# Kernel optimization log

Measured on AMD Instinct MI355X. Metric: run time of the kernel, lower is better.

Reference implementation:

```python
import jax, jax.numpy as jnp
import numpy as np

B, T, D = 32, 512, 768
K, H = 256, 512


def setup_inputs() -> dict:
    key = jax.random.key(0)
    ks = jax.random.split(key, 5)
    s = 0.02  # keep pre-activations in a sane range
    return {
        "inputs": jax.random.normal(ks[0], (B, T, D), jnp.float32),
        "W_x": jax.random.normal(ks[1], (K + 1, 4 * H), jnp.float32) * s,
        "W_h": jax.random.normal(ks[2], (H, 4 * H), jnp.float32) * s,
        "b_lstm": jnp.zeros((4 * H,), jnp.float32),
        "W_key": jax.random.normal(ks[3], (H, K), jnp.float32) * s,
        "b_key": jnp.zeros((K,), jnp.float32),
        "W_g": jax.random.normal(ks[4], (H, 1), jnp.float32) * s,
        "b_g": jnp.zeros((1,), jnp.float32),
        "conf_gain": jnp.ones((), jnp.float32),
        "conf_bias": jnp.zeros((), jnp.float32),
    }


def reference(inputs, W_x, W_h, b_lstm, W_key, b_key, W_g, b_g, conf_gain, conf_bias):
    Bq, Tq, Dq = inputs.shape
    Kq = W_key.shape[1]
    Hq = W_h.shape[0]
    t_idx = jnp.arange(Tq)
    xs = jnp.transpose(inputs, (1, 0, 2))  # [T, B, D]

    def step(carry, xt):
        t, x = xt  # t: scalar step index, x: [B, D]
        key_r, h, c, M_k, M_v = carry
        # Keras LSTMCell (gate order i, f, c, o); input is previous key_r [B, K+1]
        z = key_r @ W_x + h @ W_h + b_lstm
        i, f, g_c, o = jnp.split(z, 4, axis=-1)
        i = jax.nn.sigmoid(i)
        f = jax.nn.sigmoid(f)
        g_c = jnp.tanh(g_c)
        o = jax.nn.sigmoid(o)
        c = f * c + i * g_c
        h = o * jnp.tanh(c)  # lstm_out == hidden in Keras LSTMCell
        key_w = h @ W_key + b_key            # [B, K]
        g = jax.nn.sigmoid(h @ W_g + b_g)    # [B, 1]
        # similarity attention over all previously written memory slots
        sim = jnp.einsum('bd,tbd->bt', x, M_v)          # [B, T]
        mask = (t_idx < t)[None, :]                     # valid slots only
        w_k = jax.nn.softmax(jnp.where(mask, sim, -1e30), axis=1)
        c_k = jax.nn.sigmoid(sim * conf_gain + conf_bias)
        aug = jnp.concatenate([jnp.transpose(M_k, (1, 0, 2)), c_k[:, :, None]], axis=2)  # [B, T, K+1]
        key_r_new = jnp.where(t > 0, g * jnp.einsum('bt,btk->bk', w_k, aug), 0.0)
        M_k = M_k.at[t].set(key_w)
        M_v = M_v.at[t].set(x)
        return (key_r_new, h, c, M_k, M_v), None

    init = (
        jnp.zeros((Bq, Kq + 1), inputs.dtype),
        jnp.zeros((Bq, Hq), inputs.dtype),
        jnp.zeros((Bq, Hq), inputs.dtype),
        jnp.zeros((Tq, Bq, Kq), inputs.dtype),
        jnp.zeros((Tq, Bq, Dq), inputs.dtype),
    )
    (key_r, h, c, M_k, M_v), _ = jax.lax.scan(step, init, (t_idx, xs))
    return h  # final lstm_out
```

## Files before the change

kernel.cpp:

```cpp
#include <hip/hip_runtime.h>
#include <math.h>

#define BQ 32
#define TQ 512
#define DQ 768
#define KQ 256
#define HQ 512
#define G4 2048
#define BROW 768
#define STP 772
#define NWG 512
#define NTHR 256
#define NBG 4

typedef float f32x4 __attribute__((ext_vector_type(4)));

__device__ __forceinline__ void waitcnt0() {
  asm volatile("s_waitcnt vmcnt(0) lgkmcnt(0)" ::: "memory");
}
__device__ __forceinline__ void st_dev(float* p, float v) {
  asm volatile("global_store_dword %0, %1, off sc1" :: "v"(p), "v"(v) : "memory");
}
__device__ __forceinline__ int ld_dev(const int* p) {
  int v;
  asm volatile("global_load_dword %0, %1, off sc1\ns_waitcnt vmcnt(0)"
               : "=v"(v) : "v"(p) : "memory");
  return v;
}
__device__ __forceinline__ void wg_wait_ctr(const int* ctr, int target) {
  if (threadIdx.x < 64) {
    while (ld_dev(ctr) < target) __builtin_amdgcn_s_sleep(1);
  }
  __syncthreads();
}
__device__ __forceinline__ void wg_signal_ctr(int* ctr) {
  waitcnt0();
  __syncthreads();
  if (threadIdx.x == 0) atomicAdd(ctr, 1);
}
__device__ __forceinline__ float sigm(float x) { return 1.f / (1.f + __expf(-x)); }

__global__ void __launch_bounds__(256) gram_k(const float* __restrict__ X,
                                              float* __restrict__ Gm) {
  __shared__ __align__(16) float As[64 * 33];
  __shared__ __align__(16) float Bs[64 * 33];
  const int bid = blockIdx.x;
  const int b = blockIdx.y;
  int I = 0, base = 0;
  while (base + I + 1 <= bid) { base += I + 1; ++I; }
  const int J = bid - base;
  const int t0 = I * 64, u0 = J * 64;
  const float* Xb = X + (size_t)b * TQ * DQ;
  const int ty = threadIdx.x >> 4, tx = threadIdx.x & 15;
  const int sc = threadIdx.x & 31, sr = threadIdx.x >> 5;
  float acc[4][4];
#pragma unroll
  for (int i = 0; i < 4; ++i)
#pragma unroll
    for (int j = 0; j < 4; ++j) acc[i][j] = 0.f;
  for (int k0 = 0; k0 < DQ; k0 += 32) {
#pragma unroll
    for (int rr = 0; rr < 8; ++rr) {
      const int r = rr * 8 + sr;
      As[r * 33 + sc] = Xb[(size_t)(t0 + r) * DQ + k0 + sc];
      Bs[r * 33 + sc] = Xb[(size_t)(u0 + r) * DQ + k0 + sc];
    }
    __syncthreads();
#pragma unroll
    for (int k = 0; k < 32; ++k) {
      float av[4], bv[4];
#pragma unroll
      for (int i = 0; i < 4; ++i) av[i] = As[(ty * 4 + i) * 33 + k];
#pragma unroll
      for (int j = 0; j < 4; ++j) bv[j] = Bs[(tx * 4 + j) * 33 + k];
#pragma unroll
      for (int i = 0; i < 4; ++i)
#pragma unroll
        for (int j = 0; j < 4; ++j) acc[i][j] += av[i] * bv[j];
    }
    __syncthreads();
  }
  float* gb = Gm + (size_t)b * TQ * TQ;
#pragma unroll
  for (int i = 0; i < 4; ++i) {
    f32x4 o;
    o.x = acc[i][0]; o.y = acc[i][1]; o.z = acc[i][2]; o.w = acc[i][3];
    *(f32x4*)&gb[(size_t)(t0 + ty * 4 + i) * TQ + u0 + tx * 4] = o;
  }
}

__global__ void __launch_bounds__(256) smax_k(float* __restrict__ Gm,
                                              float* __restrict__ Sv,
                                              const float* __restrict__ cgp,
                                              const float* __restrict__ cbp) {
  const int t = blockIdx.x + 1;
  const int b = blockIdx.y;
  const int tid = threadIdx.x;
  const int lane = tid & 63;
  const int wv = tid >> 6;
  __shared__ float row[TQ];
  __shared__ float r1[4], r2[4], r3[4];
  float* R = Gm + ((size_t)b * TQ + t) * TQ;
  const float cg = cgp[0], cb = cbp[0];
  for (int i = tid; i < t; i += 256) row[i] = R[i];
  __syncthreads();
  float m = -3e38f;
  for (int i = tid; i < t; i += 256) m = fmaxf(m, row[i]);
#pragma unroll
  for (int k = 1; k < 64; k <<= 1) m = fmaxf(m, __shfl_xor(m, k));
  if (lane == 0) r1[wv] = m;
  __syncthreads();
  m = fmaxf(fmaxf(r1[0], r1[1]), fmaxf(r1[2], r1[3]));
  float s = 0.f, sck = 0.f;
  for (int i = tid; i < t; i += 256) {
    const float r = row[i];
    const float e = __expf(r - m);
    const float ck = 1.f / (1.f + __expf(-(r * cg + cb)));
    row[i] = e; s += e; sck += e * ck;
  }
#pragma unroll
  for (int k = 1; k < 64; k <<= 1) { s += __shfl_xor(s, k); sck += __shfl_xor(sck, k); }
  if (lane == 0) { r2[wv] = s; r3[wv] = sck; }
  __syncthreads();
  s = r2[0] + r2[1] + r2[2] + r2[3];
  sck = r3[0] + r3[1] + r3[2] + r3[3];
  const float inv = 1.f / s;
  for (int i = tid; i < t; i += 256) R[i] = row[i] * inv;
  if (tid == 0) Sv[(size_t)b * TQ + t] = sck * inv;
}

__global__ void __launch_bounds__(NTHR, 2) esbn_scan(
    const float* __restrict__ Wx, const float* __restrict__ Wh,
    const float* __restrict__ bl, const float* __restrict__ Wk,
    const float* __restrict__ bk, const float* __restrict__ Wg,
    const float* __restrict__ bgp, const float* __restrict__ Wmat,
    const float* __restrict__ Sv, float* buf, int* ctrs,
    float* __restrict__ out) {
  __shared__ __align__(16) float st[NBG * STP];
  __shared__ __align__(16) float wrow[NBG * TQ];
  __shared__ __align__(16) float Mk_s[16 * 520];
  __shared__ __align__(16) float wkey_s[4 * 520];
  __shared__ __align__(16) float wgv[HQ];
  __shared__ __align__(16) float svl[NBG * TQ];
  __shared__ __align__(16) float zred[4 * 8 * 4 * 4];
  __shared__ float c_s[NBG * 8];
  __shared__ float bl_s[32];
  __shared__ float bk_s[4];
  __shared__ float bg_s;

  const int tid = threadIdx.x;
  const int wg = blockIdx.x & 63;
  const int grp = blockIdx.x >> 6;
  const int b0 = grp * NBG;
  const int dc = tid >> 3;
  const int cg = tid & 7;

  int colg[4];
#pragma unroll
  for (int j = 0; j < 4; ++j) {
    const int c = cg * 4 + j;
    colg[j] = (c >> 3) * HQ + wg * 8 + (c & 7);
  }
  f32x4 wh[16], wxr[8], wxl;
#pragma unroll
  for (int i = 0; i < 16; ++i) {
    const int d = (i << 5) + dc;
    wh[i].x = Wh[(size_t)d * G4 + colg[0]];
    wh[i].y = Wh[(size_t)d * G4 + colg[1]];
    wh[i].z = Wh[(size_t)d * G4 + colg[2]];
    wh[i].w = Wh[(size_t)d * G4 + colg[3]];
  }
#pragma unroll
  for (int i = 0; i < 8; ++i) {
    const int d = (i << 5) + dc;
    wxr[i].x = Wx[(size_t)d * G4 + colg[0]];
    wxr[i].y = Wx[(size_t)d * G4 + colg[1]];
    wxr[i].z = Wx[(size_t)d * G4 + colg[2]];
    wxr[i].w = Wx[(size_t)d * G4 + colg[3]];
  }
  wxl.x = wxl.y = wxl.z = wxl.w = 0.f;
  if (dc == 0) {
    wxl.x = Wx[(size_t)256 * G4 + colg[0]];
    wxl.y = Wx[(size_t)256 * G4 + colg[1]];
    wxl.z = Wx[(size_t)256 * G4 + colg[2]];
    wxl.w = Wx[(size_t)256 * G4 + colg[3]];
  }
  for (int i = tid; i < NBG * STP; i += NTHR) st[i] = 0.f;
  for (int i = tid; i < 16 * 520; i += NTHR) Mk_s[i] = 0.f;
  for (int i = tid; i < 4 * 520; i += NTHR) {
    const int kl = i / 520, u = i - kl * 520;
    wkey_s[i] = (u < HQ) ? Wk[(size_t)u * KQ + wg * 4 + kl] : 0.f;
  }
  for (int i = tid; i < HQ; i += NTHR) wgv[i] = Wg[i];
  for (int i = tid; i < NBG * TQ; i += NTHR)
    svl[i] = Sv[(size_t)(b0 + (i >> 9)) * TQ + (i & 511)];
  if (tid < 32) bl_s[tid] = bl[(tid >> 3) * HQ + wg * 8 + (tid & 7)];
  if (tid < 4) bk_s[tid] = bk[wg * 4 + tid];
  if (tid == 0) bg_s = bgp[0];
  if (tid < NBG * 8) c_s[tid] = 0.f;
  __syncthreads();

  int* ctrH = ctrs + grp * 64;
  int* ctrA = ctrs + grp * 64 + 32;
  const int yb = tid >> 6;
  const int ykl = (tid >> 4) & 3;
  const int ytc = tid & 15;
  const int lt = tid & 63;

  for (int t = 0; t < TQ; ++t) {
    const int p = t & 1, pn = p ^ 1;
    float wv8[8];
    const bool rowv = (t >= 1) && (t < TQ - 1);
    if (rowv) {
      const float* wr = Wmat + ((size_t)(b0 + yb) * TQ + t) * TQ + lt;
#pragma unroll
      for (int k = 0; k < 8; ++k) wv8[k] = wr[k << 6];
    }
    if (t > 0) {
      wg_wait_ctr(ctrH, 64 * t);
      const float* base = buf + (size_t)(p * BQ + b0) * BROW;
      f32x4 v0, v1;
      const int i0 = tid, i1 = tid + 256;
      const float* q0 = base + ((i0 >> 7) * BROW) + ((i0 & 127) << 2);
      const float* q1 = base + ((i1 >> 7) * BROW) + ((i1 & 127) << 2);
      asm volatile("global_load_dwordx4 %0, %1, off sc1" : "=v"(v0) : "v"(q0));
      asm volatile("global_load_dwordx4 %0, %1, off sc1" : "=v"(v1) : "v"(q1));
      asm volatile("s_waitcnt vmcnt(0)" : "+v"(v0), "+v"(v1) : : "memory");
      *(f32x4*)&st[((i0 >> 7) * STP) + ((i0 & 127) << 2)] = v0;
      *(f32x4*)&st[((i1 >> 7) * STP) + ((i1 & 127) << 2)] = v1;
    }
    __syncthreads();
    f32x4 acc[NBG];
#pragma unroll
    for (int b = 0; b < NBG; ++b) { acc[b].x = acc[b].y = acc[b].z = acc[b].w = 0.f; }
#pragma unroll
    for (int i = 0; i < 16; ++i) {
      const f32x4 w = wh[i];
      const int d = (i << 5) + dc;
#pragma unroll
      for (int b = 0; b < NBG; ++b) acc[b] += st[b * STP + d] * w;
    }
    float gv[NBG];
    {
      const int sb = lt >> 4, sl = lt & 15;
      float a = 0.f;
      const float* hb = &st[sb * STP];
      const float* wb = wgv;
#pragma unroll
      for (int j = 0; j < 8; ++j) {
        const int u = sl + (j << 4) + ((j & 3) << 7);
        a += hb[u] * wb[u];
      }
      a = 0.f;
#pragma unroll
      for (int j = 0; j < 32; ++j) {
        const int u = sl + (j << 4);
        a += hb[u] * wb[u];
      }
      a += __shfl_xor(a, 1);
      a += __shfl_xor(a, 2);
      a += __shfl_xor(a, 4);
      a += __shfl_xor(a, 8);
#pragma unroll
      for (int b = 0; b < NBG; ++b) gv[b] = sigm(__shfl(a, b << 4) + bg_s);
    }
    if (t > 0) {
      wg_wait_ctr(ctrA, 64 * t);
      const float* base = buf + (size_t)(p * BQ + b0) * BROW;
      f32x4 v2;
      const float* q2 = base + ((tid >> 6) * BROW) + 512 + ((tid & 63) << 2);
      asm volatile("global_load_dwordx4 %0, %1, off sc1" : "=v"(v2) : "v"(q2));
      asm volatile("s_waitcnt vmcnt(0)" : "+v"(v2) : : "memory");
      *(f32x4*)&st[((tid >> 6) * STP) + 512 + ((tid & 63) << 2)] = v2;
    }
    __syncthreads();
    f32x4 pk[NBG];
#pragma unroll
    for (int b = 0; b < NBG; ++b) { pk[b].x = pk[b].y = pk[b].z = pk[b].w = 0.f; }
#pragma unroll
    for (int i = 0; i < 8; ++i) {
      const f32x4 w = wxr[i];
      const int d = 512 + (i << 5) + dc;
#pragma unroll
      for (int b = 0; b < NBG; ++b) pk[b] += st[b * STP + d] * w;
    }
    if (dc == 0 && t > 0) {
#pragma unroll
      for (int b = 0; b < NBG; ++b) pk[b] += svl[(b << 9) + t - 1] * wxl;
    }
#pragma unroll
    for (int b = 0; b < NBG; ++b) {
      const float g = gv[b];
      acc[b].x += g * pk[b].x; acc[b].y += g * pk[b].y;
      acc[b].z += g * pk[b].z; acc[b].w += g * pk[b].w;
    }
#pragma unroll
    for (int m = 8; m <= 32; m <<= 1) {
#pragma unroll
      for (int b = 0; b < NBG; ++b) {
        acc[b].x += __shfl_xor(acc[b].x, m);
        acc[b].y += __shfl_xor(acc[b].y, m);
        acc[b].z += __shfl_xor(acc[b].z, m);
        acc[b].w += __shfl_xor(acc[b].w, m);
      }
    }
    if (lt < 8) {
      const int wv = tid >> 6;
#pragma unroll
      for (int b = 0; b < NBG; ++b)
        *(f32x4*)&zred[((wv * 8 + lt) * 4 + b) * 4] = acc[b];
    }
    __syncthreads();
    if (tid < 32) {
      const int b = tid >> 3, u = tid & 7;
      float zg[4];
#pragma unroll
      for (int g = 0; g < 4; ++g) {
        const int cgi = g * 2 + (u >> 2), comp = u & 3;
        float z = bl_s[g * 8 + u];
#pragma unroll
        for (int wv = 0; wv < 4; ++wv) z += zred[((wv * 8 + cgi) * 4 + b) * 4 + comp];
        zg[g] = z;
      }
      const float gi = sigm(zg[0]);
      const float gf = sigm(zg[1]);
      const float go = sigm(zg[3]);
      const float cn = gf * c_s[tid] + gi * tanhf(zg[2]);
      const float hv = go * tanhf(cn);
      c_s[tid] = cn;
      if (t == TQ - 1) out[(size_t)(b0 + b) * HQ + wg * 8 + u] = hv;
      else st_dev(buf + (size_t)(pn * BQ + b0 + b) * BROW + wg * 8 + u, hv);
    }
    if (t == TQ - 1) break;
    wg_signal_ctr(ctrH);
    if (t >= 1) {
#pragma unroll
      for (int k = 0; k < 8; ++k) wrow[yb * TQ + lt + (k << 6)] = wv8[k];
      float kw = 0.f, accA = 0.f;
      const float* hrow = &st[yb * STP];
      const float* wkr = &wkey_s[ykl * 520];
      const float* mk = &Mk_s[(yb * 4 + ykl) * 520];
      const float* wb = &wrow[yb * TQ];
#pragma unroll
      for (int j = 0; j < 32; ++j) {
        const int u = ytc + (j << 4);
        kw += hrow[u] * wkr[u];
        accA += wb[u] * mk[u];
      }
#pragma unroll
      for (int m = 1; m <= 8; m <<= 1) {
        kw += __shfl_xor(kw, m);
        accA += __shfl_xor(accA, m);
      }
      kw += bk_s[ykl];
      accA += wb[t - 1] * kw;
      if (ytc == 0) {
        st_dev(buf + (size_t)(pn * BQ + b0 + yb) * BROW + 512 + wg * 4 + ykl, accA);
        Mk_s[(yb * 4 + ykl) * 520 + (t - 1)] = kw;
      }
    }
    wg_signal_ctr(ctrA);
  }
}

extern "C" void kernel_launch(void* const* d_in, const int* in_sizes, int n_in,
                              void* d_out, int out_size, void* d_ws, size_t ws_size,
                              hipStream_t stream) {
  (void)in_sizes; (void)n_in; (void)out_size; (void)ws_size;
  const float* X  = (const float*)d_in[0];
  const float* Wx = (const float*)d_in[1];
  const float* Wh = (const float*)d_in[2];
  const float* bl = (const float*)d_in[3];
  const float* Wk = (const float*)d_in[4];
  const float* bk = (const float*)d_in[5];
  const float* Wg = (const float*)d_in[6];
  const float* bg = (const float*)d_in[7];
  const float* cg = (const float*)d_in[8];
  const float* cb = (const float*)d_in[9];
  float* out = (float*)d_out;
  float* ws = (float*)d_ws;

  float* Gm = ws;
  float* Sv = ws + (size_t)8388608;
  float* buf = ws + (size_t)8404992;
  int* ctrs = (int*)(ws + (size_t)8454144);

  hipMemsetAsync(Sv, 0, (size_t)(16384 + 49152 + 512) * 4, stream);
  gram_k<<<dim3(36, BQ), dim3(256), 0, stream>>>(X, Gm);
  smax_k<<<dim3(TQ - 1, BQ), dim3(256), 0, stream>>>(Gm, Sv, cg, cb);

  void* args[] = {(void*)&Wx, (void*)&Wh, (void*)&bl, (void*)&Wk, (void*)&bk,
                  (void*)&Wg, (void*)&bg, (void*)&Gm, (void*)&Sv,
                  (void*)&buf, (void*)&ctrs, (void*)&out};
  hipError_t e = hipLaunchCooperativeKernel((const void*)esbn_scan, dim3(NWG),
                                            dim3(NTHR), args, 0, stream);
  if (e != hipSuccess) {
    esbn_scan<<<dim3(NWG), dim3(NTHR), 0, stream>>>(Wx, Wh, bl, Wk, bk, Wg, bg,
                                                    Gm, Sv, buf, ctrs, out);
  }
}
```

Baseline: 4.188 ms.

## Replace atomic counters with per-workgroup tagged publish slots for step sync

Each workgroup now writes its h and key-read outputs into its own 64-float slot, next to two tag words holding the step index. Waiters poll all 64 tags in parallel with a wave-wide check, replacing the shared atomicAdd counters. This removes atomic contention on a single counter per group and places the data next to the flag, at the cost of more polling loads and a layout remap when gathering into shared memory. It also removes a dead dot-product loop in the gate computation.

Measured after the change: 4.601 ms. +9.9%, slower.

```diff
diff --git a/kernel.cpp b/kernel.cpp
--- a/kernel.cpp
+++ b/kernel.cpp
@@ -7,11 +7,12 @@
 #define KQ 256
 #define HQ 512
 #define G4 2048
-#define BROW 768
 #define STP 772
 #define NWG 512
 #define NTHR 256
 #define NBG 4
+#define PBLK 64
+#define PGRP (2 * 64 * PBLK)
 
 typedef float f32x4 __attribute__((ext_vector_type(4)));
 
@@ -19,6 +20,9 @@
   asm volatile("s_waitcnt vmcnt(0) lgkmcnt(0)" ::: "memory");
 }
 __device__ __forceinline__ void st_dev(float* p, float v) {
+  asm volatile("global_store_dword %0, %1, off sc1" :: "v"(p), "v"(v) : "memory");
+}
+__device__ __forceinline__ void st_devi(int* p, int v) {
   asm volatile("global_store_dword %0, %1, off sc1" :: "v"(p), "v"(v) : "memory");
 }
 __device__ __forceinline__ int ld_dev(const int* p) {
@@ -27,16 +31,16 @@
                : "=v"(v) : "v"(p) : "memory");
   return v;
 }
-__device__ __forceinline__ void wg_wait_ctr(const int* ctr, int target) {
+__device__ __forceinline__ void wg_wait_tag(const int* tags, int target) {
   if (threadIdx.x < 64) {
-    while (ld_dev(ctr) < target) __builtin_amdgcn_s_sleep(1);
+    const int* p = tags + (threadIdx.x << 6);
+    for (;;) {
+      int v = ld_dev(p);
+      if (__all(v >= target)) break;
+      __builtin_amdgcn_s_sleep(1);
+    }
   }
   __syncthreads();
-}
-__device__ __forceinline__ void wg_signal_ctr(int* ctr) {
-  waitcnt0();
-  __syncthreads();
-  if (threadIdx.x == 0) atomicAdd(ctr, 1);
 }
 __device__ __forceinline__ float sigm(float x) { return 1.f / (1.f + __expf(-x)); }
 
@@ -134,8 +138,9 @@
     const float* __restrict__ bl, const float* __restrict__ Wk,
     const float* __restrict__ bk, const float* __restrict__ Wg,
     const float* __restrict__ bgp, const float* __restrict__ Wmat,
-    const float* __restrict__ Sv, float* buf, int* ctrs,
+    const float* __restrict__ Sv, float* pub, int* ctrs,
     float* __restrict__ out) {
+  (void)ctrs;
   __shared__ __align__(16) float st[NBG * STP];
   __shared__ __align__(16) float wrow[NBG * TQ];
   __shared__ __align__(16) float Mk_s[16 * 520];
@@ -200,8 +205,7 @@
   if (tid < NBG * 8) c_s[tid] = 0.f;
   __syncthreads();
 
-  int* ctrH = ctrs + grp * 64;
-  int* ctrA = ctrs + grp * 64 + 32;
+  float* pg = pub + (size_t)grp * PGRP;
   const int yb = tid >> 6;
   const int ykl = (tid >> 4) & 3;
   const int ytc = tid & 15;
@@ -209,6 +213,8 @@
 
   for (int t = 0; t < TQ; ++t) {
     const int p = t & 1, pn = p ^ 1;
+    float* pp = pg + p * (64 * PBLK);
+    float* ppn = pg + pn * (64 * PBLK);
     float wv8[8];
     const bool rowv = (t >= 1) && (t < TQ - 1);
     if (rowv) {
@@ -217,17 +223,18 @@
       for (int k = 0; k < 8; ++k) wv8[k] = wr[k << 6];
     }
     if (t > 0) {
-      wg_wait_ctr(ctrH, 64 * t);
-      const float* base = buf + (size_t)(p * BQ + b0) * BROW;
+      wg_wait_tag((const int*)pp + 48, t);
       f32x4 v0, v1;
       const int i0 = tid, i1 = tid + 256;
-      const float* q0 = base + ((i0 >> 7) * BROW) + ((i0 & 127) << 2);
-      const float* q1 = base + ((i1 >> 7) * BROW) + ((i1 & 127) << 2);
+      const int w0 = i0 >> 3, pt0 = i0 & 7;
+      const int w1 = i1 >> 3, pt1 = i1 & 7;
+      const float* q0 = pp + w0 * PBLK + (pt0 << 2);
+      const float* q1 = pp + w1 * PBLK + (pt1 << 2);
       asm volatile("global_load_dwordx4 %0, %1, off sc1" : "=v"(v0) : "v"(q0));
       asm volatile("global_load_dwordx4 %0, %1, off sc1" : "=v"(v1) : "v"(q1));
       asm volatile("s_waitcnt vmcnt(0)" : "+v"(v0), "+v"(v1) : : "memory");
-      *(f32x4*)&st[((i0 >> 7) * STP) + ((i0 & 127) << 2)] = v0;
-      *(f32x4*)&st[((i1 >> 7) * STP) + ((i1 & 127) << 2)] = v1;
+      *(f32x4*)&st[(pt0 >> 1) * STP + (w0 << 3) + ((pt0 & 1) << 2)] = v0;
+      *(f32x4*)&st[(pt1 >> 1) * STP + (w1 << 3) + ((pt1 & 1) << 2)] = v1;
     }
     __syncthreads();
     f32x4 acc[NBG];
@@ -243,19 +250,12 @@
     float gv[NBG];
     {
       const int sb = lt >> 4, sl = lt & 15;
+      const float* hb = &st[sb * STP];
       float a = 0.f;
-      const float* hb = &st[sb * STP];
-      const float* wb = wgv;
-#pragma unroll
-      for (int j = 0; j < 8; ++j) {
-        const int u = sl + (j << 4) + ((j & 3) << 7);
-        a += hb[u] * wb[u];
-      }
-      a = 0.f;
 #pragma unroll
       for (int j = 0; j < 32; ++j) {
         const int u = sl + (j << 4);
-        a += hb[u] * wb[u];
+        a += hb[u] * wgv[u];
       }
       a += __shfl_xor(a, 1);
       a += __shfl_xor(a, 2);
@@ -265,13 +265,13 @@
       for (int b = 0; b < NBG; ++b) gv[b] = sigm(__shfl(a, b << 4) + bg_s);
     }
     if (t > 0) {
-      wg_wait_ctr(ctrA, 64 * t);
-      const float* base = buf + (size_t)(p * BQ + b0) * BROW;
+      wg_wait_tag((const int*)pp + 49, t);
       f32x4 v2;
-      const float* q2 = base + ((tid >> 6) * BROW) + 512 + ((tid & 63) << 2);
+      const int w2 = tid >> 2, b2 = tid & 3;
+      const float* q2 = pp + w2 * PBLK + 32 + (b2 << 2);
       asm volatile("global_load_dwordx4 %0, %1, off sc1" : "=v"(v2) : "v"(q2));
       asm volatile("s_waitcnt vmcnt(0)" : "+v"(v2) : : "memory");
-      *(f32x4*)&st[((tid >> 6) * STP) + 512 + ((tid & 63) << 2)] = v2;
+      *(f32x4*)&st[b2 * STP + 512 + (w2 << 2)] = v2;
     }
     __syncthreads();
     f32x4 pk[NBG];
@@ -329,10 +329,12 @@
       const float hv = go * tanhf(cn);
       c_s[tid] = cn;
       if (t == TQ - 1) out[(size_t)(b0 + b) * HQ + wg * 8 + u] = hv;
-      else st_dev(buf + (size_t)(pn * BQ + b0 + b) * BROW + wg * 8 + u, hv);
+      else st_dev(ppn + wg * PBLK + tid, hv);
     }
     if (t == TQ - 1) break;
-    wg_signal_ctr(ctrH);
+    waitcnt0();
+    __syncthreads();
+    if (tid == 0) st_devi((int*)ppn + wg * PBLK + 48, t + 1);
     if (t >= 1) {
 #pragma unroll
       for (int k = 0; k < 8; ++k) wrow[yb * TQ + lt + (k << 6)] = wv8[k];
@@ -355,11 +357,13 @@
       kw += bk_s[ykl];
       accA += wb[t - 1] * kw;
       if (ytc == 0) {
-        st_dev(buf + (size_t)(pn * BQ + b0 + yb) * BROW + 512 + wg * 4 + ykl, accA);
+        st_dev(ppn + wg * PBLK + 32 + (yb << 2) + ykl, accA);
         Mk_s[(yb * 4 + ykl) * 520 + (t - 1)] = kw;
       }
     }
-    wg_signal_ctr(ctrA);
+    waitcnt0();
+    __syncthreads();
+    if (tid == 0) st_devi((int*)ppn + wg * PBLK + 49, t + 1);
   }
 }
 
@@ -382,20 +386,20 @@
 
   float* Gm = ws;
   float* Sv = ws + (size_t)8388608;
-  float* buf = ws + (size_t)8404992;
-  int* ctrs = (int*)(ws + (size_t)8454144);
-
-  hipMemsetAsync(Sv, 0, (size_t)(16384 + 49152 + 512) * 4, stream);
+  float* pub = ws + (size_t)8404992;
+  int* ctrs = nullptr;
+
+  hipMemsetAsync(Sv, 0, (size_t)(16384 + 65536) * 4, stream);
   gram_k<<<dim3(36, BQ), dim3(256), 0, stream>>>(X, Gm);
   smax_k<<<dim3(TQ - 1, BQ), dim3(256), 0, stream>>>(Gm, Sv, cg, cb);
 
   void* args[] = {(void*)&Wx, (void*)&Wh, (void*)&bl, (void*)&Wk, (void*)&bk,
                   (void*)&Wg, (void*)&bg, (void*)&Gm, (void*)&Sv,
-                  (void*)&buf, (void*)&ctrs, (void*)&out};
+                  (void*)&pub, (void*)&ctrs, (void*)&out};
   hipError_t e = hipLaunchCooperativeKernel((const void*)esbn_scan, dim3(NWG),
                                             dim3(NTHR), args, 0, stream);
   if (e != hipSuccess) {
     esbn_scan<<<dim3(NWG), dim3(NTHR), 0, stream>>>(Wx, Wh, bl, Wk, bk, Wg, bg,
-                                                    Gm, Sv, buf, ctrs, out);
-  }
-}
+                                                    Gm, Sv, pub, ctrs, out);
+  }
+}
```

## Poll key counter early, prefetch key_r slice, and drop signal barrier

Applied to the files above, without the earlier changes.

While the first wave is already waiting on the h-row loads, it also checks the second (key_r) counter. If that data is ready, the key_r slice is loaded before the W_h matvec runs, so its latency overlaps compute instead of a second wait-and-load. The ctrH signal no longer does a full-workgroup waitcnt plus __syncthreads; only the first wave, which holds the global h stores, drains and increments the counter. A dead duplicate reduction loop in the gate computation is also removed. This relies on only threads below 64 issuing the cross-workgroup stores before the signal.

After: 4.219 ms. About the same (+0.7%).

```diff
diff --git a/kernel.cpp b/kernel.cpp
--- a/kernel.cpp
+++ b/kernel.cpp
@@ -15,9 +15,6 @@
 
 typedef float f32x4 __attribute__((ext_vector_type(4)));
 
-__device__ __forceinline__ void waitcnt0() {
-  asm volatile("s_waitcnt vmcnt(0) lgkmcnt(0)" ::: "memory");
-}
 __device__ __forceinline__ void st_dev(float* p, float v) {
   asm volatile("global_store_dword %0, %1, off sc1" :: "v"(p), "v"(v) : "memory");
 }
@@ -34,7 +31,7 @@
   __syncthreads();
 }
 __device__ __forceinline__ void wg_signal_ctr(int* ctr) {
-  waitcnt0();
+  asm volatile("s_waitcnt vmcnt(0) lgkmcnt(0)" ::: "memory");
   __syncthreads();
   if (threadIdx.x == 0) atomicAdd(ctr, 1);
 }
@@ -147,6 +144,7 @@
   __shared__ float bl_s[32];
   __shared__ float bk_s[4];
   __shared__ float bg_s;
+  __shared__ int aflag_s;
 
   const int tid = threadIdx.x;
   const int wg = blockIdx.x & 63;
@@ -216,6 +214,10 @@
 #pragma unroll
       for (int k = 0; k < 8; ++k) wv8[k] = wr[k << 6];
     }
+    f32x4 vA;
+    vA.x = vA.y = vA.z = vA.w = 0.f;
+    const float* qA = buf + (size_t)(p * BQ + b0) * BROW +
+                      ((tid >> 6) * BROW) + 512 + ((tid & 63) << 2);
     if (t > 0) {
       wg_wait_ctr(ctrH, 64 * t);
       const float* base = buf + (size_t)(p * BQ + b0) * BROW;
@@ -225,11 +227,21 @@
       const float* q1 = base + ((i1 >> 7) * BROW) + ((i1 & 127) << 2);
       asm volatile("global_load_dwordx4 %0, %1, off sc1" : "=v"(v0) : "v"(q0));
       asm volatile("global_load_dwordx4 %0, %1, off sc1" : "=v"(v1) : "v"(q1));
+      if (tid < 64) {
+        const int av = ld_dev(ctrA);
+        if (tid == 0) aflag_s = (av >= 64 * t);
+      }
       asm volatile("s_waitcnt vmcnt(0)" : "+v"(v0), "+v"(v1) : : "memory");
       *(f32x4*)&st[((i0 >> 7) * STP) + ((i0 & 127) << 2)] = v0;
       *(f32x4*)&st[((i1 >> 7) * STP) + ((i1 & 127) << 2)] = v1;
+    } else if (tid == 0) {
+      aflag_s = 0;
     }
     __syncthreads();
+    const int aEarly = aflag_s;
+    if (t > 0 && aEarly) {
+      asm volatile("global_load_dwordx4 %0, %1, off sc1" : "=v"(vA) : "v"(qA));
+    }
     f32x4 acc[NBG];
 #pragma unroll
     for (int b = 0; b < NBG; ++b) { acc[b].x = acc[b].y = acc[b].z = acc[b].w = 0.f; }
@@ -243,19 +255,12 @@
     float gv[NBG];
     {
       const int sb = lt >> 4, sl = lt & 15;
+      const float* hb = &st[sb * STP];
       float a = 0.f;
-      const float* hb = &st[sb * STP];
-      const float* wb = wgv;
-#pragma unroll
-      for (int j = 0; j < 8; ++j) {
-        const int u = sl + (j << 4) + ((j & 3) << 7);
-        a += hb[u] * wb[u];
-      }
-      a = 0.f;
 #pragma unroll
       for (int j = 0; j < 32; ++j) {
         const int u = sl + (j << 4);
-        a += hb[u] * wb[u];
+        a += hb[u] * wgv[u];
       }
       a += __shfl_xor(a, 1);
       a += __shfl_xor(a, 2);
@@ -265,13 +270,12 @@
       for (int b = 0; b < NBG; ++b) gv[b] = sigm(__shfl(a, b << 4) + bg_s);
     }
     if (t > 0) {
-      wg_wait_ctr(ctrA, 64 * t);
-      const float* base = buf + (size_t)(p * BQ + b0) * BROW;
-      f32x4 v2;
-      const float* q2 = base + ((tid >> 6) * BROW) + 512 + ((tid & 63) << 2);
-      asm volatile("global_load_dwordx4 %0, %1, off sc1" : "=v"(v2) : "v"(q2));
-      asm volatile("s_waitcnt vmcnt(0)" : "+v"(v2) : : "memory");
-      *(f32x4*)&st[((tid >> 6) * STP) + 512 + ((tid & 63) << 2)] = v2;
+      if (!aEarly) {
+        wg_wait_ctr(ctrA, 64 * t);
+        asm volatile("global_load_dwordx4 %0, %1, off sc1" : "=v"(vA) : "v"(qA));
+      }
+      asm volatile("s_waitcnt vmcnt(0)" : "+v"(vA) : : "memory");
+      *(f32x4*)&st[((tid >> 6) * STP) + 512 + ((tid & 63) << 2)] = vA;
     }
     __syncthreads();
     f32x4 pk[NBG];
@@ -332,7 +336,10 @@
       else st_dev(buf + (size_t)(pn * BQ + b0 + b) * BROW + wg * 8 + u, hv);
     }
     if (t == TQ - 1) break;
-    wg_signal_ctr(ctrH);
+    if (tid < 64) {
+      asm volatile("s_waitcnt vmcnt(0)" ::: "memory");
+      if (tid == 0) atomicAdd(ctrH, 1);
+    }
     if (t >= 1) {
 #pragma unroll
       for (int k = 0; k < 8; ++k) wrow[yb * TQ + lt + (k << 6)] = wv8[k];
```

## Repartition scan to 2 batches x 32 workgroups per group with wider column slices

Applied to the files above, without the earlier changes.

Changes the persistent scan's work split from 8 groups of 64 workgroups each handling 4 batch rows to 16 groups of 32 workgroups each handling 2 batch rows. Each workgroup now owns 16 hidden columns and 8 key columns, which doubles the register-resident weights per thread. The change also narrows the h-ready signal so only the first wave waits on its stores. Smaller groups mean fewer participants in each per-step global counter barrier and less per-step shared-memory traffic. The cost is higher register pressure and more per-workgroup arithmetic, since each weight is reused across only 2 batches instead of 4.

After: 8.394 ms. 100% more time.

```diff
diff --git a/kernel.cpp b/kernel.cpp
--- a/kernel.cpp
+++ b/kernel.cpp
@@ -11,13 +11,11 @@
 #define STP 772
 #define NWG 512
 #define NTHR 256
-#define NBG 4
+#define NBG 2
+#define GW 32
 
 typedef float f32x4 __attribute__((ext_vector_type(4)));
 
-__device__ __forceinline__ void waitcnt0() {
-  asm volatile("s_waitcnt vmcnt(0) lgkmcnt(0)" ::: "memory");
-}
 __device__ __forceinline__ void st_dev(float* p, float v) {
   asm volatile("global_store_dword %0, %1, off sc1" :: "v"(p), "v"(v) : "memory");
 }
@@ -34,7 +32,7 @@
   __syncthreads();
 }
 __device__ __forceinline__ void wg_signal_ctr(int* ctr) {
-  waitcnt0();
+  asm volatile("s_waitcnt vmcnt(0) lgkmcnt(0)" ::: "memory");
   __syncthreads();
   if (threadIdx.x == 0) atomicAdd(ctr, 1);
 }
@@ -137,125 +135,114 @@
     const float* __restrict__ Sv, float* buf, int* ctrs,
     float* __restrict__ out) {
   __shared__ __align__(16) float st[NBG * STP];
-  __shared__ __align__(16) float wrow[NBG * TQ];
+  __shared__ __align__(16) float wrow[4 * TQ];
   __shared__ __align__(16) float Mk_s[16 * 520];
-  __shared__ __align__(16) float wkey_s[4 * 520];
+  __shared__ __align__(16) float wkey_s[8 * 520];
   __shared__ __align__(16) float wgv[HQ];
   __shared__ __align__(16) float svl[NBG * TQ];
-  __shared__ __align__(16) float zred[4 * 8 * 4 * 4];
-  __shared__ float c_s[NBG * 8];
-  __shared__ float bl_s[32];
-  __shared__ float bk_s[4];
+  __shared__ __align__(16) float zred[4 * 16 * NBG * 4];
+  __shared__ float c_s[NBG * 16];
+  __shared__ float bl_s[64];
+  __shared__ float bk_s[8];
   __shared__ float bg_s;
 
   const int tid = threadIdx.x;
-  const int wg = blockIdx.x & 63;
-  const int grp = blockIdx.x >> 6;
+  const int wg = blockIdx.x & 31;
+  const int grp = blockIdx.x >> 5;
   const int b0 = grp * NBG;
-  const int dc = tid >> 3;
-  const int cg = tid & 7;
+  const int dc = tid >> 4;
+  const int cg = tid & 15;
 
   int colg[4];
 #pragma unroll
   for (int j = 0; j < 4; ++j) {
     const int c = cg * 4 + j;
-    colg[j] = (c >> 3) * HQ + wg * 8 + (c & 7);
-  }
-  f32x4 wh[16], wxr[8], wxl;
-#pragma unroll
-  for (int i = 0; i < 16; ++i) {
-    const int d = (i << 5) + dc;
+    colg[j] = (c >> 4) * HQ + wg * 16 + (c & 15);
+  }
+  f32x4 wh[32], wxr[16], wxl;
+#pragma unroll
+  for (int i = 0; i < 32; ++i) {
+    const int d = (i << 4) + dc;
     wh[i].x = Wh[(size_t)d * G4 + colg[0]];
     wh[i].y = Wh[(size_t)d * G4 + colg[1]];
     wh[i].z = Wh[(size_t)d * G4 + colg[2]];
     wh[i].w = Wh[(size_t)d * G4 + colg[3]];
   }
 #pragma unroll
-  for (int i = 0; i < 8; ++i) {
-    const int d = (i << 5) + dc;
+  for (int i = 0; i < 16; ++i) {
+    const int d = (i << 4) + dc;
     wxr[i].x = Wx[(size_t)d * G4 + colg[0]];
     wxr[i].y = Wx[(size_t)d * G4 + colg[1]];
     wxr[i].z = Wx[(size_t)d * G4 + colg[2]];
     wxr[i].w = Wx[(size_t)d * G4 + colg[3]];
   }
-  wxl.x = wxl.y = wxl.z = wxl.w = 0.f;
-  if (dc == 0) {
-    wxl.x = Wx[(size_t)256 * G4 + colg[0]];
-    wxl.y = Wx[(size_t)256 * G4 + colg[1]];
-    wxl.z = Wx[(size_t)256 * G4 + colg[2]];
-    wxl.w = Wx[(size_t)256 * G4 + colg[3]];
-  }
+  wxl.x = Wx[(size_t)256 * G4 + colg[0]];
+  wxl.y = Wx[(size_t)256 * G4 + colg[1]];
+  wxl.z = Wx[(size_t)256 * G4 + colg[2]];
+  wxl.w = Wx[(size_t)256 * G4 + colg[3]];
+
   for (int i = tid; i < NBG * STP; i += NTHR) st[i] = 0.f;
   for (int i = tid; i < 16 * 520; i += NTHR) Mk_s[i] = 0.f;
-  for (int i = tid; i < 4 * 520; i += NTHR) {
+  for (int i = tid; i < 8 * 520; i += NTHR) {
     const int kl = i / 520, u = i - kl * 520;
-    wkey_s[i] = (u < HQ) ? Wk[(size_t)u * KQ + wg * 4 + kl] : 0.f;
+    wkey_s[i] = (u < HQ) ? Wk[(size_t)u * KQ + wg * 8 + kl] : 0.f;
   }
   for (int i = tid; i < HQ; i += NTHR) wgv[i] = Wg[i];
   for (int i = tid; i < NBG * TQ; i += NTHR)
     svl[i] = Sv[(size_t)(b0 + (i >> 9)) * TQ + (i & 511)];
-  if (tid < 32) bl_s[tid] = bl[(tid >> 3) * HQ + wg * 8 + (tid & 7)];
-  if (tid < 4) bk_s[tid] = bk[wg * 4 + tid];
+  if (tid < 64) bl_s[tid] = bl[(tid >> 4) * HQ + wg * 16 + (tid & 15)];
+  if (tid < 8) bk_s[tid] = bk[wg * 8 + tid];
   if (tid == 0) bg_s = bgp[0];
-  if (tid < NBG * 8) c_s[tid] = 0.f;
+  if (tid < NBG * 16) c_s[tid] = 0.f;
   __syncthreads();
 
   int* ctrH = ctrs + grp * 64;
   int* ctrA = ctrs + grp * 64 + 32;
-  const int yb = tid >> 6;
-  const int ykl = (tid >> 4) & 3;
+  const int wv0 = tid >> 6;
+  const int yb2 = tid >> 7;
+  const int lt = tid & 63;
+  const int row = tid >> 4;
   const int ytc = tid & 15;
-  const int lt = tid & 63;
 
   for (int t = 0; t < TQ; ++t) {
     const int p = t & 1, pn = p ^ 1;
     float wv8[8];
     const bool rowv = (t >= 1) && (t < TQ - 1);
     if (rowv) {
-      const float* wr = Wmat + ((size_t)(b0 + yb) * TQ + t) * TQ + lt;
+      const float* wr = Wmat + ((size_t)(b0 + yb2) * TQ + t) * TQ + lt;
 #pragma unroll
       for (int k = 0; k < 8; ++k) wv8[k] = wr[k << 6];
     }
     if (t > 0) {
-      wg_wait_ctr(ctrH, 64 * t);
+      wg_wait_ctr(ctrH, GW * t);
       const float* base = buf + (size_t)(p * BQ + b0) * BROW;
-      f32x4 v0, v1;
-      const int i0 = tid, i1 = tid + 256;
-      const float* q0 = base + ((i0 >> 7) * BROW) + ((i0 & 127) << 2);
-      const float* q1 = base + ((i1 >> 7) * BROW) + ((i1 & 127) << 2);
+      f32x4 v0;
+      const int hb = tid >> 7, off = (tid & 127) << 2;
+      const float* q0 = base + hb * BROW + off;
       asm volatile("global_load_dwordx4 %0, %1, off sc1" : "=v"(v0) : "v"(q0));
-      asm volatile("global_load_dwordx4 %0, %1, off sc1" : "=v"(v1) : "v"(q1));
-      asm volatile("s_waitcnt vmcnt(0)" : "+v"(v0), "+v"(v1) : : "memory");
-      *(f32x4*)&st[((i0 >> 7) * STP) + ((i0 & 127) << 2)] = v0;
-      *(f32x4*)&st[((i1 >> 7) * STP) + ((i1 & 127) << 2)] = v1;
+      asm volatile("s_waitcnt vmcnt(0)" : "+v"(v0) : : "memory");
+      *(f32x4*)&st[hb * STP + off] = v0;
     }
     __syncthreads();
     f32x4 acc[NBG];
 #pragma unroll
     for (int b = 0; b < NBG; ++b) { acc[b].x = acc[b].y = acc[b].z = acc[b].w = 0.f; }
 #pragma unroll
-    for (int i = 0; i < 16; ++i) {
+    for (int i = 0; i < 32; ++i) {
       const f32x4 w = wh[i];
-      const int d = (i << 5) + dc;
+      const int d = (i << 4) + dc;
 #pragma unroll
       for (int b = 0; b < NBG; ++b) acc[b] += st[b * STP + d] * w;
     }
     float gv[NBG];
     {
-      const int sb = lt >> 4, sl = lt & 15;
+      const int sb = (lt >> 4) & 1, sl = lt & 15;
+      const float* hb = &st[sb * STP];
       float a = 0.f;
-      const float* hb = &st[sb * STP];
-      const float* wb = wgv;
-#pragma unroll
-      for (int j = 0; j < 8; ++j) {
-        const int u = sl + (j << 4) + ((j & 3) << 7);
-        a += hb[u] * wb[u];
-      }
-      a = 0.f;
 #pragma unroll
       for (int j = 0; j < 32; ++j) {
         const int u = sl + (j << 4);
-        a += hb[u] * wb[u];
+        a += hb[u] * wgv[u];
       }
       a += __shfl_xor(a, 1);
       a += __shfl_xor(a, 2);
@@ -265,22 +252,25 @@
       for (int b = 0; b < NBG; ++b) gv[b] = sigm(__shfl(a, b << 4) + bg_s);
     }
     if (t > 0) {
-      wg_wait_ctr(ctrA, 64 * t);
-      const float* base = buf + (size_t)(p * BQ + b0) * BROW;
-      f32x4 v2;
-      const float* q2 = base + ((tid >> 6) * BROW) + 512 + ((tid & 63) << 2);
-      asm volatile("global_load_dwordx4 %0, %1, off sc1" : "=v"(v2) : "v"(q2));
-      asm volatile("s_waitcnt vmcnt(0)" : "+v"(v2) : : "memory");
-      *(f32x4*)&st[((tid >> 6) * STP) + 512 + ((tid & 63) << 2)] = v2;
+      wg_wait_ctr(ctrA, GW * t);
+      if (tid < 128) {
+        const float* base = buf + (size_t)(p * BQ + b0) * BROW;
+        f32x4 v2;
+        const int ab = tid >> 6, off2 = (tid & 63) << 2;
+        const float* q2 = base + ab * BROW + 512 + off2;
+        asm volatile("global_load_dwordx4 %0, %1, off sc1" : "=v"(v2) : "v"(q2));
+        asm volatile("s_waitcnt vmcnt(0)" : "+v"(v2) : : "memory");
+        *(f32x4*)&st[ab * STP + 512 + off2] = v2;
+      }
     }
     __syncthreads();
     f32x4 pk[NBG];
 #pragma unroll
     for (int b = 0; b < NBG; ++b) { pk[b].x = pk[b].y = pk[b].z = pk[b].w = 0.f; }
 #pragma unroll
-    for (int i = 0; i < 8; ++i) {
+    for (int i = 0; i < 16; ++i) {
       const f32x4 w = wxr[i];
-      const int d = 512 + (i << 5) + dc;
+      const int d = 512 + (i << 4) + dc;
 #pragma unroll
       for (int b = 0; b < NBG; ++b) pk[b] += st[b * STP + d] * w;
     }
@@ -295,7 +285,7 @@
       acc[b].z += g * pk[b].z; acc[b].w += g * pk[b].w;
     }
 #pragma unroll
-    for (int m = 8; m <= 32; m <<= 1) {
+    for (int m = 16; m <= 32; m <<= 1) {
 #pragma unroll
       for (int b = 0; b < NBG; ++b) {
         acc[b].x += __shfl_xor(acc[b].x, m);
@@ -304,22 +294,21 @@
         acc[b].w += __shfl_xor(acc[b].w, m);
       }
     }
-    if (lt < 8) {
-      const int wv = tid >> 6;
+    if (lt < 16) {
 #pragma unroll
       for (int b = 0; b < NBG; ++b)
-        *(f32x4*)&zred[((wv * 8 + lt) * 4 + b) * 4] = acc[b];
+        *(f32x4*)&zred[((wv0 * 16 + lt) * NBG + b) * 4] = acc[b];
     }
     __syncthreads();
     if (tid < 32) {
-      const int b = tid >> 3, u = tid & 7;
+      const int b = tid >> 4, u = tid & 15;
       float zg[4];
 #pragma unroll
       for (int g = 0; g < 4; ++g) {
-        const int cgi = g * 2 + (u >> 2), comp = u & 3;
-        float z = bl_s[g * 8 + u];
-#pragma unroll
-        for (int wv = 0; wv < 4; ++wv) z += zred[((wv * 8 + cgi) * 4 + b) * 4 + comp];
+        const int cgi = g * 4 + (u >> 2), comp = u & 3;
+        float z = bl_s[g * 16 + u];
+#pragma unroll
+        for (int w = 0; w < 4; ++w) z += zred[((w * 16 + cgi) * NBG + b) * 4 + comp];
         zg[g] = z;
       }
       const float gi = sigm(zg[0]);
@@ -328,35 +317,39 @@
       const float cn = gf * c_s[tid] + gi * tanhf(zg[2]);
       const float hv = go * tanhf(cn);
       c_s[tid] = cn;
-      if (t == TQ - 1) out[(size_t)(b0 + b) * HQ + wg * 8 + u] = hv;
-      else st_dev(buf + (size_t)(pn * BQ + b0 + b) * BROW + wg * 8 + u, hv);
+      if (t == TQ - 1) out[(size_t)(b0 + b) * HQ + wg * 16 + u] = hv;
+      else st_dev(buf + (size_t)(pn * BQ + b0 + b) * BROW + wg * 16 + u, hv);
     }
     if (t == TQ - 1) break;
-    wg_signal_ctr(ctrH);
+    if (tid < 64) {
+      asm volatile("s_waitcnt vmcnt(0)" ::: "memory");
+      if (tid == 0) atomicAdd(ctrH, 1);
+    }
     if (t >= 1) {
-#pragma unroll
-      for (int k = 0; k < 8; ++k) wrow[yb * TQ + lt + (k << 6)] = wv8[k];
+      float* wrw = &wrow[wv0 * TQ];
+#pragma unroll
+      for (int k = 0; k < 8; ++k) wrw[lt + (k << 6)] = wv8[k];
+      const int b = row >> 3, kl = row & 7;
       float kw = 0.f, accA = 0.f;
-      const float* hrow = &st[yb * STP];
-      const float* wkr = &wkey_s[ykl * 520];
-      const float* mk = &Mk_s[(yb * 4 + ykl) * 520];
-      const float* wb = &wrow[yb * TQ];
+      const float* hrow = &st[b * STP];
+      const float* wkr = &wkey_s[kl * 520];
+      const float* mk = &Mk_s[row * 520];
 #pragma unroll
       for (int j = 0; j < 32; ++j) {
         const int u = ytc + (j << 4);
         kw += hrow[u] * wkr[u];
-        accA += wb[u] * mk[u];
+        accA += wrw[u] * mk[u];
       }
 #pragma unroll
       for (int m = 1; m <= 8; m <<= 1) {
         kw += __shfl_xor(kw, m);
         accA += __shfl_xor(accA, m);
       }
-      kw += bk_s[ykl];
-      accA += wb[t - 1] * kw;
+      kw += bk_s[kl];
+      accA += wrw[t - 1] * kw;
       if (ytc == 0) {
-        st_dev(buf + (size_t)(pn * BQ + b0 + yb) * BROW + 512 + wg * 4 + ykl, accA);
-        Mk_s[(yb * 4 + ykl) * 520 + (t - 1)] = kw;
+        st_dev(buf + (size_t)(pn * BQ + b0 + b) * BROW + 512 + wg * 8 + kl, accA);
+        Mk_s[row * 520 + (t - 1)] = kw;
       }
     }
     wg_signal_ctr(ctrA);
@@ -385,7 +378,7 @@
   float* buf = ws + (size_t)8404992;
   int* ctrs = (int*)(ws + (size_t)8454144);
 
-  hipMemsetAsync(Sv, 0, (size_t)(16384 + 49152 + 512) * 4, stream);
+  hipMemsetAsync(Sv, 0, (size_t)(16384 + 49152 + 1024) * 4, stream);
   gram_k<<<dim3(36, BQ), dim3(256), 0, stream>>>(X, Gm);
   smax_k<<<dim3(TQ - 1, BQ), dim3(256), 0, stream>>>(Gm, Sv, cg, cb);
 
```
